# Kernel optimization log

Measured on AMD Instinct MI355X. Metric: run time of the kernel, lower is better.

The kernel has to match this reference:

```python
import jax, jax.numpy as jnp
import numpy as np

D_MODEL = 1024
N_HEADS = 16
DH = (D_MODEL // N_HEADS) // 2  # depth // 2 = 32
B, S = 4, 2048


def setup_inputs() -> dict:
    key = jax.random.key(0)
    ks = jax.random.split(key, 8)
    scale_in = 1.0
    q = jax.random.normal(ks[0], (B, S, D_MODEL), dtype=jnp.float32)
    k = jax.random.normal(ks[1], (B, S, D_MODEL), dtype=jnp.float32)
    v = jax.random.normal(ks[2], (B, S, D_MODEL), dtype=jnp.float32)
    # Per-head projection weights stacked over the head axis (glorot-ish init)
    w_std = (2.0 / (D_MODEL + DH)) ** 0.5
    Wq = jax.random.normal(ks[3], (N_HEADS, D_MODEL, DH), dtype=jnp.float32) * w_std
    Wk = jax.random.normal(ks[4], (N_HEADS, D_MODEL, DH), dtype=jnp.float32) * w_std
    Wv = jax.random.normal(ks[5], (N_HEADS, D_MODEL, DH), dtype=jnp.float32) * w_std
    wo_std = (2.0 / (N_HEADS * DH + D_MODEL)) ** 0.5
    Wo = jax.random.normal(ks[6], (N_HEADS * DH, D_MODEL), dtype=jnp.float32) * wo_std
    return {"q": q, "k": k, "v": v, "Wq": Wq, "Wk": Wk, "Wv": Wv, "Wo": Wo}


def reference(q, k, v, Wq, Wk, Wv, Wo):
    # NOTE: source scales by d_model**-0.5 (not head_dim**-0.5)
    scale = D_MODEL ** (-0.5)
    Q = jnp.einsum("bsd,hde->bhse", q, Wq)   # [B,H,S,DH]
    K = jnp.einsum("btd,hde->bhte", k, Wk)
    V = jnp.einsum("btd,hde->bhte", v, Wv)
    attn = jnp.einsum("bhse,bhte->bhst", Q, K) * scale  # [B,H,S,S]
    attn = jax.nn.softmax(attn, axis=-1)
    x = jnp.einsum("bhst,bhte->bhse", attn, V)  # [B,H,S,DH]
    # concat heads along feature dim (head order = concat order in source)
    x = jnp.transpose(x, (0, 2, 1, 3)).reshape(q.shape[0], q.shape[1], N_HEADS * DH)
    return x @ Wo  # [B,S,D_MODEL]; dropout is identity (training=False)
```

## Files before the change

### kernel.cpp

```cpp
#include <hip/hip_runtime.h>
#include <hip/hip_bf16.h>

typedef __attribute__((ext_vector_type(8))) short short8;
typedef __attribute__((ext_vector_type(4))) float f32x4;
typedef __attribute__((ext_vector_type(4))) float fv4;
typedef __attribute__((ext_vector_type(4))) unsigned int u32x4;

#define MFMA16(a, b, c) __builtin_amdgcn_mfma_f32_16x16x32_bf16((a), (b), (c), 0, 0, 0)
#define SBAR() __builtin_amdgcn_sched_barrier(0)
#define RBAR() __builtin_amdgcn_s_barrier()

typedef const __attribute__((address_space(1))) unsigned int gu32;
typedef __attribute__((address_space(3))) unsigned int lu32;

__device__ __forceinline__ short f2b(float f) {
  unsigned int x = __builtin_bit_cast(unsigned int, f);
  x += 0x7fffu + ((x >> 16) & 1u);
  return (short)(x >> 16);
}

__device__ __forceinline__ unsigned int cvtpk(float lo, float hi) {
  unsigned int r;
  asm("v_cvt_pk_bf16_f32 %0, %1, %2" : "=v"(r) : "v"(lo), "v"(hi));
  return r;
}

#define hexp2(x) __builtin_amdgcn_exp2f(x)

__global__ void prep_weights(const float* __restrict__ Wq, const float* __restrict__ Wk,
                             const float* __restrict__ Wv, const float* __restrict__ Wo,
                             short* __restrict__ WqT, short* __restrict__ WkT,
                             short* __restrict__ WvT, short* __restrict__ WoT) {
  const float SC2 = 0.045084220027780106f;
  int idx = blockIdx.x * 256 + threadIdx.x;
  if (idx < 3 * 512 * 1024) {
    int wsel = idx >> 19;
    int rem = idx & ((1 << 19) - 1);
    int n = rem >> 10;
    int d = rem & 1023;
    const float* W = (wsel == 0) ? Wq : ((wsel == 1) ? Wk : Wv);
    short* WT = (wsel == 0) ? WqT : ((wsel == 1) ? WkT : WvT);
    float v = W[(n >> 5) * (1024 * 32) + d * 32 + (n & 31)];
    if (wsel == 0) v *= SC2;
    WT[n * 1024 + d] = f2b(v);
  } else {
    int idx2 = idx - 3 * 512 * 1024;
    int n = idx2 >> 9;
    int kk = idx2 & 511;
    WoT[n * 512 + kk] = f2b(Wo[kk * 1024 + n]);
  }
}

__global__ __launch_bounds__(256, 2) void proj_gemm(
    const float* __restrict__ q, const float* __restrict__ k, const float* __restrict__ v,
    const short* __restrict__ BTall,
    short* __restrict__ Qb, short* __restrict__ Kb, short* __restrict__ Vtb) {
  __shared__ char smem[73728];
  const int tid = threadIdx.x;
  const int lane = tid & 63;
  const int w = tid >> 6;
  const int l15 = lane & 15, g = lane >> 4;
  const int wm = (w >> 1) * 64, wn = (w & 1) * 64;
  const int id = blockIdx.x;
  const int bm = id & 63;
  const int bn = id >> 6;
  const int zz = bn >> 2;
  const int bnz = bn & 3;
  const float* Az = (zz == 0) ? q : ((zz == 1) ? k : v);
  const short* BT = BTall + (size_t)zz * 512 * 1024;
  const int bm0 = bm * 128, bn0z = bnz * 128;

  const int ar = lane >> 3;
  const int au = lane & 7;
  const int br = lane >> 2;
  const int bu = lane & 3;

  f32x4 zf = {0.f, 0.f, 0.f, 0.f};
  f32x4 acc[4][4];
#pragma unroll
  for (int a = 0; a < 4; ++a)
#pragma unroll
    for (int bq = 0; bq < 4; ++bq) acc[a][bq] = zf;

#define STAGE(base, k0)                                                          \
  {                                                                              \
    _Pragma("unroll") for (int i = 0; i < 2; ++i) {                              \
      int rowa = 32 * w + 8 * i + ar;                                            \
      __builtin_amdgcn_global_load_lds(                                          \
          (gu32*)(Az + (size_t)(bm0 + rowa) * 1024 + (k0) + 4 * (au ^ (rowa & 7))), \
          (lu32*)(smem + (base) + w * 4096 + i * 1024), 16, 0, 0);               \
      int rowa2 = 32 * w + 8 * (i + 2) + ar;                                     \
      __builtin_amdgcn_global_load_lds(                                          \
          (gu32*)(Az + (size_t)(bm0 + rowa2) * 1024 + (k0) + 4 * (au ^ (rowa2 & 7))), \
          (lu32*)(smem + (base) + w * 4096 + (i + 2) * 1024), 16, 0, 0);         \
      int rowb = 32 * w + 16 * i + br;                                           \
      __builtin_amdgcn_global_load_lds(                                          \
          (gu32*)(BT + (size_t)(bn0z + rowb) * 1024 + (k0) +                     \
                  8 * (bu ^ ((rowb >> 1) & 3))),                                 \
          (lu32*)(smem + (base) + 16384 + w * 2048 + i * 1024), 16, 0, 0);       \
    }                                                                            \
  }

#define COMPUTE(base)                                                          \
  {                                                                            \
    short8 af[4], bfr[4];                                                      \
    _Pragma("unroll") for (int nf = 0; nf < 4; ++nf) {                         \
      int row = wn + nf * 16 + l15;                                            \
      bfr[nf] = *(const short8*)(smem + (base) + 16384 + row * 64 +            \
                                 ((g ^ ((row >> 1) & 3)) * 16));               \
    }                                                                          \
    _Pragma("unroll") for (int mf = 0; mf < 4; ++mf) {                         \
      int row = wm + mf * 16 + l15;                                            \
      fv4 a0 = *(const fv4*)(smem + (base) + row * 128 +                       \
                             (((2 * g) ^ (row & 7)) * 16));                    \
      fv4 a1 = *(const fv4*)(smem + (base) + row * 128 +                       \
                             (((2 * g + 1) ^ (row & 7)) * 16));                \
      u32x4 wv;                                                                \
      wv[0] = cvtpk(a0[0], a0[1]);                                             \
      wv[1] = cvtpk(a0[2], a0[3]);                                             \
      wv[2] = cvtpk(a1[0], a1[1]);                                             \
      wv[3] = cvtpk(a1[2], a1[3]);                                             \
      af[mf] = __builtin_bit_cast(short8, wv);                                 \
    }                                                                          \
    __builtin_amdgcn_s_setprio(1);                                             \
    _Pragma("unroll") for (int mf = 0; mf < 4; ++mf)                           \
        _Pragma("unroll") for (int nf = 0; nf < 4; ++nf)                       \
            acc[mf][nf] = MFMA16(af[mf], bfr[nf], acc[mf][nf]);                \
    __builtin_amdgcn_s_setprio(0);                                             \
  }

#define PBODY(s_, cb_, nb_)                                 \
  {                                                         \
    STAGE(nb_, ((s_) + 2) * 32);                            \
    SBAR();                                                 \
    asm volatile("s_waitcnt vmcnt(12)" ::: "memory");       \
    SBAR();                                                 \
    RBAR();                                                 \
    COMPUTE(cb_);                                           \
    RBAR();                                                 \
  }

  STAGE(0, 0);
  STAGE(24576, 32);

  for (int s = 0; s < 30; s += 3) {
    PBODY(s, 0, 49152);
    PBODY(s + 1, 24576, 0);
    PBODY(s + 2, 49152, 24576);
  }
  SBAR();
  asm volatile("s_waitcnt vmcnt(6)" ::: "memory");
  SBAR();
  RBAR();
  COMPUTE(0);
  RBAR();
  SBAR();
  asm volatile("s_waitcnt vmcnt(0)" ::: "memory");
  SBAR();
  RBAR();
  COMPUTE(24576);
  RBAR();
#undef STAGE
#undef COMPUTE
#undef PBODY

#pragma unroll
  for (int mf = 0; mf < 4; ++mf)
#pragma unroll
    for (int nf = 0; nf < 4; ++nf)
#pragma unroll
      for (int i = 0; i < 4; ++i) {
        int row = bm0 + wm + mf * 16 + g * 4 + i;
        int col = bn0z + wn + nf * 16 + l15;
        int bb = row >> 11, ss = row & 2047;
        int hh = col >> 5, ee = col & 31;
        short val = f2b(acc[mf][nf][i]);
        if (zz == 2)
          Vtb[((size_t)(bb * 16 + hh) * 32 + ee) * 2048 + ss] = val;
        else if (zz == 1)
          Kb[((size_t)(bb * 16 + hh) * 2048 + ss) * 32 + ee] = val;
        else
          Qb[((size_t)(bb * 16 + hh) * 2048 + ss) * 32 + ee] = val;
      }
}

__global__ __launch_bounds__(256, 2) void out_gemm(const short* __restrict__ X,
                                                   const short* __restrict__ WoT,
                                                   float* __restrict__ out) {
  __shared__ char smem[49152];
  const int tid = threadIdx.x;
  const int lane = tid & 63;
  const int w = tid >> 6;
  const int l15 = lane & 15, g = lane >> 4;
  const int wm = (w >> 1) * 64, wn = (w & 1) * 64;
  const int id = blockIdx.x;
  const int bm0 = (id & 63) * 128, bn0 = (id >> 6) * 128;

  const int br = lane >> 2;
  const int bu = lane & 3;

  f32x4 zf = {0.f, 0.f, 0.f, 0.f};
  f32x4 acc[4][4];
#pragma unroll
  for (int a = 0; a < 4; ++a)
#pragma unroll
    for (int bq = 0; bq < 4; ++bq) acc[a][bq] = zf;

#define STAGE(base, k0)                                                        \
  {                                                                            \
    _Pragma("unroll") for (int i = 0; i < 2; ++i) {                            \
      int row = 32 * w + 16 * i + br;                                          \
      __builtin_amdgcn_global_load_lds(                                        \
          (gu32*)(X + (size_t)(bm0 + row) * 512 + (k0) +                       \
                  8 * (bu ^ ((row >> 1) & 3))),                                \
          (lu32*)(smem + (base) + w * 2048 + i * 1024), 16, 0, 0);             \
      __builtin_amdgcn_global_load_lds(                                        \
          (gu32*)(WoT + (size_t)(bn0 + row) * 512 + (k0) +                     \
                  8 * (bu ^ ((row >> 1) & 3))),                                \
          (lu32*)(smem + (base) + 8192 + w * 2048 + i * 1024), 16, 0, 0);      \
    }                                                                          \
  }

#define COMPUTE(base)                                                          \
  {                                                                            \
    short8 af[4], bfr[4];                                                      \
    _Pragma("unroll") for (int mf = 0; mf < 4; ++mf) {                         \
      int row = wm + mf * 16 + l15;                                            \
      af[mf] = *(const short8*)(smem + (base) + row * 64 +                     \
                                ((g ^ ((row >> 1) & 3)) * 16));                \
    }                                                                          \
    _Pragma("unroll") for (int nf = 0; nf < 4; ++nf) {                         \
      int row = wn + nf * 16 + l15;                                            \
      bfr[nf] = *(const short8*)(smem + (base) + 8192 + row * 64 +             \
                                 ((g ^ ((row >> 1) & 3)) * 16));               \
    }                                                                          \
    __builtin_amdgcn_s_setprio(1);                                             \
    _Pragma("unroll") for (int mf = 0; mf < 4; ++mf)                           \
        _Pragma("unroll") for (int nf = 0; nf < 4; ++nf)                       \
            acc[mf][nf] = MFMA16(af[mf], bfr[nf], acc[mf][nf]);                \
    __builtin_amdgcn_s_setprio(0);                                             \
  }

#define PBODY(s_, cb_, nb_)                                 \
  {                                                         \
    STAGE(nb_, ((s_) + 2) * 32);                            \
    SBAR();                                                 \
    asm volatile("s_waitcnt vmcnt(8)" ::: "memory");        \
    SBAR();                                                 \
    RBAR();                                                 \
    COMPUTE(cb_);                                           \
    RBAR();                                                 \
  }

  STAGE(0, 0);
  STAGE(16384, 32);
  for (int s = 0; s < 12; s += 3) {
    PBODY(s, 0, 32768);
    PBODY(s + 1, 16384, 0);
    PBODY(s + 2, 32768, 16384);
  }
  PBODY(12, 0, 32768);
  PBODY(13, 16384, 0);
  SBAR();
  asm volatile("s_waitcnt vmcnt(4)" ::: "memory");
  SBAR();
  RBAR();
  COMPUTE(32768);
  RBAR();
  SBAR();
  asm volatile("s_waitcnt vmcnt(0)" ::: "memory");
  SBAR();
  RBAR();
  COMPUTE(0);
  RBAR();
#undef STAGE
#undef COMPUTE
#undef PBODY

#pragma unroll
  for (int mf = 0; mf < 4; ++mf)
#pragma unroll
    for (int nf = 0; nf < 4; ++nf)
#pragma unroll
      for (int i = 0; i < 4; ++i) {
        int row = bm0 + wm + mf * 16 + g * 4 + i;
        int col = bn0 + wn + nf * 16 + l15;
        out[(size_t)row * 1024 + col] = acc[mf][nf][i];
      }
}

__device__ __forceinline__ void qk_half(short8 k0, short8 k1, short8 k2, short8 k3,
                                        short8 qf, const f32x4& zf,
                                        short8& pf0, short8& pf1) {
  f32x4 s0 = MFMA16(k0, qf, zf);
  f32x4 s1 = MFMA16(k1, qf, zf);
  f32x4 s2 = MFMA16(k2, qf, zf);
  f32x4 s3 = MFMA16(k3, qf, zf);
#pragma unroll
  for (int i = 0; i < 4; ++i) {
    s0[i] = hexp2(s0[i]);
    s1[i] = hexp2(s1[i]);
    s2[i] = hexp2(s2[i]);
    s3[i] = hexp2(s3[i]);
  }
  u32x4 w0, w1;
  w0[0] = cvtpk(s0[0], s0[1]);
  w0[1] = cvtpk(s0[2], s0[3]);
  w0[2] = cvtpk(s1[0], s1[1]);
  w0[3] = cvtpk(s1[2], s1[3]);
  w1[0] = cvtpk(s2[0], s2[1]);
  w1[1] = cvtpk(s2[2], s2[3]);
  w1[2] = cvtpk(s3[0], s3[1]);
  w1[3] = cvtpk(s3[2], s3[3]);
  pf0 = __builtin_bit_cast(short8, w0);
  pf1 = __builtin_bit_cast(short8, w1);
}

__global__ __launch_bounds__(256, 4) void attn(const short* __restrict__ Qb,
                                               const short* __restrict__ Kb,
                                               const short* __restrict__ Vtb,
                                               short* __restrict__ X) {
  __shared__ short KV[2][2][2048];
  const int tid = threadIdx.x;
  const int lane = tid & 63;
  const int w = tid >> 6;
  const int l15 = lane & 15, g = lane >> 4;
  const int id = blockIdx.x;
  const int bh = id & 63;
  const int qblk = id >> 6;
  const int bb = bh >> 4, hh = bh & 15;
  const int q0 = qblk * 128 + w * 32;

  const short* Qp = Qb + ((size_t)bh * 2048 + q0) * 32;
  const short* Kp = Kb + (size_t)bh * 2048 * 32;
  const short* Vp = Vtb + (size_t)bh * 32 * 2048;

  short8 qfA = *(const short8*)(Qp + l15 * 32 + g * 8);
  short8 qfB = *(const short8*)(Qp + (16 + l15) * 32 + g * 8);

  const int kbase = 8 * (l15 >> 2) + (l15 & 3);
  const int koff = (w & 1) * 4 + (w >> 1) * 32;
  const int vrow = (w >> 1) * 16;
  const int vcol = (w & 1) * 32;
  const short* Ksrc0 = Kp + (size_t)(kbase + koff) * 32 + g * 8;
  const short* Vsrc0 = Vp + (size_t)(l15 + vrow) * 2048 + vcol + g * 8;

  f32x4 zf = {0.f, 0.f, 0.f, 0.f};
  f32x4 o_loA = zf, o_hiA = zf, o_loB = zf, o_hiB = zf;
  f32x4 accLA = zf, accLB = zf;
  u32x4 ones_u = {0x3F803F80u, 0x3F803F80u, 0x3F803F80u, 0x3F803F80u};
  const short8 ones = __builtin_bit_cast(short8, ones_u);

#define STAGE(b, t0)                                                        \
  {                                                                         \
    __builtin_amdgcn_global_load_lds((gu32*)(Ksrc0 + (size_t)(t0) * 32),    \
                                     (lu32*)&KV[b][0][w * 512], 16, 0, 0);  \
    __builtin_amdgcn_global_load_lds((gu32*)(Vsrc0 + (t0)),                 \
                                     (lu32*)&KV[b][1][w * 512], 16, 0, 0);  \
  }

#define BODY(b)                                                       \
  {                                                                   \
    short8 k0 = *(const short8*)(&KV[b][0][0 * 512 + lane * 8]);      \
    short8 k1 = *(const short8*)(&KV[b][0][1 * 512 + lane * 8]);      \
    short8 k2 = *(const short8*)(&KV[b][0][2 * 512 + lane * 8]);      \
    short8 k3 = *(const short8*)(&KV[b][0][3 * 512 + lane * 8]);      \
    short8 vlo0 = *(const short8*)(&KV[b][1][0 * 512 + lane * 8]);    \
    short8 vlo1 = *(const short8*)(&KV[b][1][1 * 512 + lane * 8]);    \
    short8 vhi0 = *(const short8*)(&KV[b][1][2 * 512 + lane * 8]);    \
    short8 vhi1 = *(const short8*)(&KV[b][1][3 * 512 + lane * 8]);    \
    short8 pfA0, pfA1, pfB0, pfB1;                                    \
    qk_half(k0, k1, k2, k3, qfA, zf, pfA0, pfA1);                     \
    qk_half(k0, k1, k2, k3, qfB, zf, pfB0, pfB1);                     \
    __builtin_amdgcn_s_setprio(1);                                    \
    accLA = MFMA16(pfA0, ones, accLA);                                \
    accLA = MFMA16(pfA1, ones, accLA);                                \
    accLB = MFMA16(pfB0, ones, accLB);                                \
    accLB = MFMA16(pfB1, ones, accLB);                                \
    o_loA = MFMA16(pfA0, vlo0, o_loA);                                \
    o_loA = MFMA16(pfA1, vlo1, o_loA);                                \
    o_hiA = MFMA16(pfA0, vhi0, o_hiA);                                \
    o_hiA = MFMA16(pfA1, vhi1, o_hiA);                                \
    o_loB = MFMA16(pfB0, vlo0, o_loB);                                \
    o_loB = MFMA16(pfB1, vlo1, o_loB);                                \
    o_hiB = MFMA16(pfB0, vhi0, o_hiB);                                \
    o_hiB = MFMA16(pfB1, vhi1, o_hiB);                                \
    __builtin_amdgcn_s_setprio(0);                                    \
  }

  STAGE(0, 0);
  __syncthreads();
  for (int t0 = 0; t0 < 2048; t0 += 128) {
    STAGE(1, t0 + 64);
    BODY(0);
    __syncthreads();
    if (t0 + 128 < 2048) {
      STAGE(0, t0 + 128);
    }
    BODY(1);
    __syncthreads();
  }
#undef STAGE
#undef BODY

#pragma unroll
  for (int i = 0; i < 4; ++i) {
    float invA = 1.0f / accLA[i];
    float invB = 1.0f / accLB[i];
    int ssA = q0 + 4 * g + i;
    size_t baseA = ((size_t)bb * 2048 + ssA) * 512 + hh * 32;
    X[baseA + l15] = f2b(o_loA[i] * invA);
    X[baseA + 16 + l15] = f2b(o_hiA[i] * invA);
    size_t baseB = baseA + (size_t)16 * 512;
    X[baseB + l15] = f2b(o_loB[i] * invB);
    X[baseB + 16 + l15] = f2b(o_hiB[i] * invB);
  }
}

extern "C" void kernel_launch(void* const* d_in, const int* in_sizes, int n_in,
                              void* d_out, int out_size, void* d_ws, size_t ws_size,
                              hipStream_t stream) {
  const float* q = (const float*)d_in[0];
  const float* k = (const float*)d_in[1];
  const float* v = (const float*)d_in[2];
  const float* Wq = (const float*)d_in[3];
  const float* Wk = (const float*)d_in[4];
  const float* Wv = (const float*)d_in[5];
  const float* Wo = (const float*)d_in[6];

  char* ws = (char*)d_ws;
  const size_t MB = 1u << 20;
  short* WqT = (short*)(ws + 0 * MB);
  short* WkT = (short*)(ws + 1 * MB);
  short* WvT = (short*)(ws + 2 * MB);
  short* WoT = (short*)(ws + 3 * MB);
  short* Qb  = (short*)(ws + 4 * MB);
  short* Kb  = (short*)(ws + 12 * MB);
  short* Vtb = (short*)(ws + 20 * MB);
  short* Xb  = (short*)(ws + 28 * MB);

  prep_weights<<<8192, 256, 0, stream>>>(Wq, Wk, Wv, Wo, WqT, WkT, WvT, WoT);
  proj_gemm<<<768, 256, 0, stream>>>(q, k, v, WqT, Qb, Kb, Vtb);
  attn<<<1024, 256, 0, stream>>>(Qb, Kb, Vtb, Xb);
  out_gemm<<<512, 256, 0, stream>>>(Xb, WoT, (float*)d_out);
}
```

Baseline: 122.6 us.

## Enlarge projection GEMM tiles to 256x256 with 512-thread blocks and double buffering

The projection GEMM now uses 256x256 output tiles per block with 8 waves, each wave computing 128x64, in place of 128x128 tiles with 4 waves. The aim is more reuse of each loaded A/B tile and less global traffic per FLOP. The triple-buffered pipeline is replaced by double buffering with one stage of prefetch, and MFMAs are interleaved per A fragment. The grid shrinks to 192 blocks, which is below the CU count of the device, so occupancy and latency hiding may suffer. Register pressure from 32 accumulators per lane also rises.

```diff
diff --git a/kernel.cpp b/kernel.cpp
--- a/kernel.cpp
+++ b/kernel.cpp
@@ -51,24 +51,26 @@
   }
 }
 
-__global__ __launch_bounds__(256, 2) void proj_gemm(
+__global__ __launch_bounds__(512, 2) void proj_gemm(
     const float* __restrict__ q, const float* __restrict__ k, const float* __restrict__ v,
     const short* __restrict__ BTall,
     short* __restrict__ Qb, short* __restrict__ Kb, short* __restrict__ Vtb) {
-  __shared__ char smem[73728];
+  __shared__ char smem[98304];
   const int tid = threadIdx.x;
   const int lane = tid & 63;
   const int w = tid >> 6;
   const int l15 = lane & 15, g = lane >> 4;
-  const int wm = (w >> 1) * 64, wn = (w & 1) * 64;
+  const int wm = (w >> 2) * 128;
+  const int wn = (w & 3) * 64;
   const int id = blockIdx.x;
-  const int bm = id & 63;
-  const int bn = id >> 6;
-  const int zz = bn >> 2;
-  const int bnz = bn & 3;
+  const int mblk = id & 31;
+  const int nblk = id >> 5;
+  const int zz = nblk >> 1;
+  const int bnz = nblk & 1;
   const float* Az = (zz == 0) ? q : ((zz == 1) ? k : v);
   const short* BT = BTall + (size_t)zz * 512 * 1024;
-  const int bm0 = bm * 128, bn0z = bnz * 128;
+  const int bm0 = mblk * 256;
+  const int bn0z = bnz * 256;
 
   const int ar = lane >> 3;
   const int au = lane & 7;
@@ -76,40 +78,38 @@
   const int bu = lane & 3;
 
   f32x4 zf = {0.f, 0.f, 0.f, 0.f};
-  f32x4 acc[4][4];
-#pragma unroll
-  for (int a = 0; a < 4; ++a)
+  f32x4 acc[8][4];
+#pragma unroll
+  for (int a = 0; a < 8; ++a)
 #pragma unroll
     for (int bq = 0; bq < 4; ++bq) acc[a][bq] = zf;
 
 #define STAGE(base, k0)                                                          \
   {                                                                              \
-    _Pragma("unroll") for (int i = 0; i < 2; ++i) {                              \
-      int rowa = 32 * w + 8 * i + ar;                                            \
+    _Pragma("unroll") for (int c = 0; c < 4; ++c) {                              \
+      int rowa = 32 * w + 8 * c + ar;                                            \
       __builtin_amdgcn_global_load_lds(                                          \
           (gu32*)(Az + (size_t)(bm0 + rowa) * 1024 + (k0) + 4 * (au ^ (rowa & 7))), \
-          (lu32*)(smem + (base) + w * 4096 + i * 1024), 16, 0, 0);               \
-      int rowa2 = 32 * w + 8 * (i + 2) + ar;                                     \
-      __builtin_amdgcn_global_load_lds(                                          \
-          (gu32*)(Az + (size_t)(bm0 + rowa2) * 1024 + (k0) + 4 * (au ^ (rowa2 & 7))), \
-          (lu32*)(smem + (base) + w * 4096 + (i + 2) * 1024), 16, 0, 0);         \
+          (lu32*)(smem + (base) + w * 4096 + c * 1024), 16, 0, 0);               \
+    }                                                                            \
+    _Pragma("unroll") for (int i = 0; i < 2; ++i) {                              \
       int rowb = 32 * w + 16 * i + br;                                           \
       __builtin_amdgcn_global_load_lds(                                          \
           (gu32*)(BT + (size_t)(bn0z + rowb) * 1024 + (k0) +                     \
                   8 * (bu ^ ((rowb >> 1) & 3))),                                 \
-          (lu32*)(smem + (base) + 16384 + w * 2048 + i * 1024), 16, 0, 0);       \
+          (lu32*)(smem + (base) + 32768 + w * 2048 + i * 1024), 16, 0, 0);       \
     }                                                                            \
   }
 
 #define COMPUTE(base)                                                          \
   {                                                                            \
-    short8 af[4], bfr[4];                                                      \
+    short8 bfr[4];                                                             \
     _Pragma("unroll") for (int nf = 0; nf < 4; ++nf) {                         \
       int row = wn + nf * 16 + l15;                                            \
-      bfr[nf] = *(const short8*)(smem + (base) + 16384 + row * 64 +            \
+      bfr[nf] = *(const short8*)(smem + (base) + 32768 + row * 64 +            \
                                  ((g ^ ((row >> 1) & 3)) * 16));               \
     }                                                                          \
-    _Pragma("unroll") for (int mf = 0; mf < 4; ++mf) {                         \
+    _Pragma("unroll") for (int mf = 0; mf < 8; ++mf) {                         \
       int row = wm + mf * 16 + l15;                                            \
       fv4 a0 = *(const fv4*)(smem + (base) + row * 128 +                       \
                              (((2 * g) ^ (row & 7)) * 16));                    \
@@ -120,52 +120,35 @@
       wv[1] = cvtpk(a0[2], a0[3]);                                             \
       wv[2] = cvtpk(a1[0], a1[1]);                                             \
       wv[3] = cvtpk(a1[2], a1[3]);                                             \
-      af[mf] = __builtin_bit_cast(short8, wv);                                 \
+      short8 af = __builtin_bit_cast(short8, wv);                              \
+      __builtin_amdgcn_s_setprio(1);                                           \
+      _Pragma("unroll") for (int nf = 0; nf < 4; ++nf)                         \
+          acc[mf][nf] = MFMA16(af, bfr[nf], acc[mf][nf]);                      \
+      __builtin_amdgcn_s_setprio(0);                                           \
     }                                                                          \
-    __builtin_amdgcn_s_setprio(1);                                             \
-    _Pragma("unroll") for (int mf = 0; mf < 4; ++mf)                           \
-        _Pragma("unroll") for (int nf = 0; nf < 4; ++nf)                       \
-            acc[mf][nf] = MFMA16(af[mf], bfr[nf], acc[mf][nf]);                \
-    __builtin_amdgcn_s_setprio(0);                                             \
-  }
-
-#define PBODY(s_, cb_, nb_)                                 \
-  {                                                         \
-    STAGE(nb_, ((s_) + 2) * 32);                            \
-    SBAR();                                                 \
-    asm volatile("s_waitcnt vmcnt(12)" ::: "memory");       \
-    SBAR();                                                 \
-    RBAR();                                                 \
-    COMPUTE(cb_);                                           \
-    RBAR();                                                 \
   }
 
   STAGE(0, 0);
-  STAGE(24576, 32);
-
-  for (int s = 0; s < 30; s += 3) {
-    PBODY(s, 0, 49152);
-    PBODY(s + 1, 24576, 0);
-    PBODY(s + 2, 49152, 24576);
-  }
-  SBAR();
-  asm volatile("s_waitcnt vmcnt(6)" ::: "memory");
-  SBAR();
-  RBAR();
-  COMPUTE(0);
-  RBAR();
-  SBAR();
-  asm volatile("s_waitcnt vmcnt(0)" ::: "memory");
-  SBAR();
-  RBAR();
-  COMPUTE(24576);
-  RBAR();
+  for (int s = 0; s < 32; ++s) {
+    const int cb = (s & 1) * 49152;
+    const int nb = ((s + 1) & 1) * 49152;
+    if (s + 1 < 32) {
+      STAGE(nb, (s + 1) * 32);
+      SBAR();
+      asm volatile("s_waitcnt vmcnt(6)" ::: "memory");
+    } else {
+      asm volatile("s_waitcnt vmcnt(0)" ::: "memory");
+    }
+    SBAR();
+    RBAR();
+    COMPUTE(cb);
+    RBAR();
+  }
 #undef STAGE
 #undef COMPUTE
-#undef PBODY
-
-#pragma unroll
-  for (int mf = 0; mf < 4; ++mf)
+
+#pragma unroll
+  for (int mf = 0; mf < 8; ++mf)
 #pragma unroll
     for (int nf = 0; nf < 4; ++nf)
 #pragma unroll
@@ -440,7 +423,7 @@
   short* Xb  = (short*)(ws + 28 * MB);
 
   prep_weights<<<8192, 256, 0, stream>>>(Wq, Wk, Wv, Wo, WqT, WkT, WvT, WoT);
-  proj_gemm<<<768, 256, 0, stream>>>(q, k, v, WqT, Qb, Kb, Vtb);
+  proj_gemm<<<192, 512, 0, stream>>>(q, k, v, WqT, Qb, Kb, Vtb);
   attn<<<1024, 256, 0, stream>>>(Qb, Kb, Vtb, Xb);
   out_gemm<<<512, 256, 0, stream>>>(Xb, WoT, (float*)d_out);
 }
```

After: 136.8 us. 11.5% more time.
